# Optimization experiments

Hardware: AMD Instinct MI355X
Metric: run time of the kernel (lower is better)

The kernel has to match this reference:

```python
import jax, jax.numpy as jnp
import numpy as np

D_MODEL = 1024
N_HEADS = 16
D_K = D_MODEL // N_HEADS
MAX_REL = 128
SEQ = 1024
BATCH = 4


def setup_inputs() -> dict:
    key = jax.random.key(0)
    ks = jax.random.split(key, 8)
    x = jax.random.normal(ks[0], (SEQ, BATCH, D_MODEL), dtype=jnp.float32)
    # nn.Linear weights: shape (out, in), applied as x @ W.T
    w_q = jax.random.normal(ks[1], (D_MODEL, D_MODEL), dtype=jnp.float32) * (1.0 / np.sqrt(D_MODEL))
    w_k = jax.random.normal(ks[2], (D_MODEL, D_MODEL), dtype=jnp.float32) * (1.0 / np.sqrt(D_MODEL))
    w_v = jax.random.normal(ks[3], (D_MODEL, D_MODEL), dtype=jnp.float32) * (1.0 / np.sqrt(D_MODEL))
    w_o = jax.random.normal(ks[4], (D_MODEL, D_MODEL), dtype=jnp.float32) * (1.0 / np.sqrt(D_MODEL))
    b_o = jnp.zeros((D_MODEL,), dtype=jnp.float32)
    rel_k = jax.random.normal(ks[5], (2 * MAX_REL + 1, D_K), dtype=jnp.float32)
    rel_v = jax.random.normal(ks[6], (2 * MAX_REL + 1, D_K), dtype=jnp.float32)
    return {"x": x, "w_q": w_q, "w_k": w_k, "w_v": w_v, "w_o": w_o, "b_o": b_o,
            "rel_k": rel_k, "rel_v": rel_v}


def _relative_positions(seq_len: int) -> jnp.ndarray:
    pos = jnp.arange(seq_len)
    rel = pos[:, None] - pos[None, :]
    rel = jnp.clip(rel, -MAX_REL, MAX_REL) + MAX_REL
    return rel  # [s, t] int indices into relative tables


def reference(x, w_q, w_k, w_v, w_o, b_o, rel_k, rel_v):
    seq_len, batch, _ = x.shape
    scale = 1.0 / np.sqrt(D_K)
    Q = (x @ w_q.T).reshape(seq_len, batch, N_HEADS, D_K)
    K = (x @ w_k.T).reshape(seq_len, batch, N_HEADS, D_K)
    V = (x @ w_v.T).reshape(seq_len, batch, N_HEADS, D_K)

    rel_idx = _relative_positions(seq_len)          # [s, t]
    rk = rel_k[rel_idx]                              # [s, t, d_k]
    rv = rel_v[rel_idx]                              # [s, t, d_k]

    scores = jnp.einsum('sbhd,tbhd->sbth', Q, K) * scale
    scores = scores + jnp.einsum('sbhd,std->sbth', Q, rk) * scale
    # NOTE: original torch code softmaxes over dim=-1 of [s,b,t,h], i.e. the
    # head axis; reproduced faithfully here.
    attn = jax.nn.softmax(scores, axis=-1)           # [s, b, t, h]

    out = jnp.einsum('sbth,tbhd->sbhd', attn, V)
    out = out + jnp.einsum('sbth,std->sbhd', attn, rv)
    out = out.reshape(seq_len, batch, D_MODEL)
    return out @ w_o.T + b_o
```

## Files before the change

kernel.cpp:

```cpp
#include <hip/hip_runtime.h>
#include <stdint.h>

#define DI __device__ __forceinline__

typedef __attribute__((ext_vector_type(8))) short bfx8;
typedef __attribute__((ext_vector_type(4))) short bfx4;
typedef __attribute__((ext_vector_type(4))) float f4;

DI unsigned short f2bf(float x){
  unsigned u = __float_as_uint(x);
  u = (u + 0x7FFFu + ((u >> 16) & 1u)) >> 16;
  return (unsigned short)u;
}
DI float bf2f(unsigned short h){ return __uint_as_float(((unsigned)h) << 16); }

DI f4 mfma32(bfx8 a, bfx8 b, f4 c){
  return __builtin_amdgcn_mfma_f32_16x16x32_bf16(a, b, c, 0, 0, 0);
}
#if __has_builtin(__builtin_amdgcn_mfma_f32_16x16x16bf16_1k)
DI f4 mfma16(bfx4 a, bfx4 b, f4 c){
  return __builtin_amdgcn_mfma_f32_16x16x16bf16_1k(a, b, c, 0, 0, 0);
}
#else
DI f4 mfma16(bfx4 a, bfx4 b, f4 c){
  f4 d = c;
  asm volatile("v_mfma_f32_16x16x16_bf16 %0, %1, %2, %0" : "+v"(d) : "v"(a), "v"(b));
  return d;
}
#endif

DI bfx4 lo4(bfx8 v){ bfx4 r; r[0]=v[0]; r[1]=v[1]; r[2]=v[2]; r[3]=v[3]; return r; }
DI bfx4 hi4(bfx8 v){ bfx4 r; r[0]=v[4]; r[1]=v[5]; r[2]=v[6]; r[3]=v[7]; return r; }

DI void gload16(const void* g, void* l){
  __builtin_amdgcn_global_load_lds(
      (__attribute__((address_space(1))) void*)g,
      (__attribute__((address_space(3))) void*)l, 16, 0, 0);
}


__global__ void k_cast(const float* __restrict__ src, unsigned short* __restrict__ dst, int n4){
  int i = blockIdx.x*256 + threadIdx.x;
  if (i < n4){
    const float4 v = ((const float4*)src)[i];
    bfx4 o;
    o[0] = (short)f2bf(v.x); o[1] = (short)f2bf(v.y);
    o[2] = (short)f2bf(v.z); o[3] = (short)f2bf(v.w);
    *(bfx4*)(dst + (size_t)i*4) = o;
  }
}

__global__ void k_castw(const float* __restrict__ s0, const float* __restrict__ s1,
                        const float* __restrict__ s2, const float* __restrict__ s3,
                        unsigned short* __restrict__ dst){
  int i = blockIdx.x*256 + threadIdx.x;
  const float* src = (blockIdx.y==0) ? s0 : (blockIdx.y==1) ? s1 : (blockIdx.y==2) ? s2 : s3;
  const float4 v = ((const float4*)src)[i];
  bfx4 o;
  o[0] = (short)f2bf(v.x); o[1] = (short)f2bf(v.y);
  o[2] = (short)f2bf(v.z); o[3] = (short)f2bf(v.w);
  *(bfx4*)(dst + (size_t)blockIdx.y*1048576 + (size_t)i*4) = o;
}

__global__ void k_relprep(const float* __restrict__ rlk, const float* __restrict__ rlv,
                          unsigned short* __restrict__ relk_bf, unsigned short* __restrict__ relvT_bf){
  int i = blockIdx.x*256 + threadIdx.x;
  if (i < 272*64){
    int r = i >> 6, d = i & 63;
    relk_bf[i] = (r < 257) ? f2bf(rlk[r*64 + d]) : (unsigned short)0;
  }
  if (i < 64*288){
    int d = i / 288, r = i % 288;
    relvT_bf[i] = (r < 257) ? f2bf(rlv[(size_t)r*64 + d]) : (unsigned short)0;
  }
}

__global__ __launch_bounds__(256, 3) void k_qkv(
    const unsigned short* __restrict__ xbf, const unsigned short* __restrict__ wqkv,
    unsigned short* __restrict__ Qf, unsigned short* __restrict__ Kf,
    unsigned short* __restrict__ Vf)
{
  __shared__ __align__(16) unsigned short smem[2][8192];
  const int nt = blockIdx.x;
  const int b  = blockIdx.y;
  const int st = blockIdx.z;
  const int w = threadIdx.x >> 6, lane = threadIdx.x & 63;
  const int wr = w >> 1, wc = w & 1;
  const int p = lane & 15, g = lane >> 4;
  const int s0 = st*128;
  const int n0 = nt*128;
  const f4 fz = {0.f,0.f,0.f,0.f};
  f4 acc[4][4];
#pragma unroll
  for (int m=0;m<4;++m)
#pragma unroll
    for (int n=0;n<4;++n) acc[m][n] = fz;

  const int j0 = w*2, j1 = w*2 + 1;
  const unsigned short* gA = xbf  + (size_t)((s0 + p)*4 + b)*1024 + g*8;
  const unsigned short* gB = wqkv + (size_t)(n0 + p)*1024 + g*8;

  {
    unsigned short* d0 = &smem[0][0];
    gload16(gA + (size_t)j0*65536, d0 + j0*512);
    gload16(gA + (size_t)j1*65536, d0 + j1*512);
    gload16(gB + (size_t)j0*16384, d0 + 4096 + j0*512);
    gload16(gB + (size_t)j1*16384, d0 + 4096 + j1*512);
  }

  for (int it=0; it<32; ++it){
    const int cur = it & 1;
    if (it < 31){
      const int kn = (it+1)*32;
      unsigned short* dn = &smem[cur^1][0];
      gload16(gA + (size_t)j0*65536 + kn, dn + j0*512);
      gload16(gA + (size_t)j1*65536 + kn, dn + j1*512);
      gload16(gB + (size_t)j0*16384 + kn, dn + 4096 + j0*512);
      gload16(gB + (size_t)j1*16384 + kn, dn + 4096 + j1*512);
      asm volatile("s_waitcnt vmcnt(4)" ::: "memory");
    } else {
      asm volatile("s_waitcnt vmcnt(0)" ::: "memory");
    }
    __builtin_amdgcn_sched_barrier(0);
    __builtin_amdgcn_s_barrier();
    __builtin_amdgcn_sched_barrier(0);
    {
      const unsigned short* Ab = &smem[cur][0];
      bfx8 af[4], bfr[4];
#pragma unroll
      for (int m=0;m<4;++m) af[m] = *(const bfx8*)(Ab + (wr*4+m)*512 + lane*8);
#pragma unroll
      for (int n=0;n<4;++n) bfr[n] = *(const bfx8*)(Ab + 4096 + (wc*4+n)*512 + lane*8);
#pragma unroll
      for (int m=0;m<4;++m)
#pragma unroll
        for (int n=0;n<4;++n)
          acc[m][n] = mfma32(af[m], bfr[n], acc[m][n]);
    }
    __builtin_amdgcn_sched_barrier(0);
    __builtin_amdgcn_s_barrier();
    __builtin_amdgcn_sched_barrier(0);
  }

  const int n64 = n0 + wc*64;
  const int sec = n64 >> 10;
  const int h = (n64 & 1023) >> 6;
  float* es = (float*)&smem[0][0] + w*1280;

  if (sec < 2){
    const float scl = (sec == 0) ? 0.125f : 1.0f;
    unsigned short* dst = (sec == 0) ? Qf : Kf;
#pragma unroll
    for (int m=0;m<4;++m){
#pragma unroll
      for (int n=0;n<4;++n)
#pragma unroll
        for (int r=0;r<4;++r)
          es[(4*g + r)*80 + 16*n + p] = acc[m][n][r] * scl;
      __syncthreads();
      f4 v0 = *(const f4*)&es[p*80 + 8*g];
      f4 v1 = *(const f4*)&es[p*80 + 8*g + 4];
      f4 v2 = *(const f4*)&es[p*80 + 32 + 8*g];
      f4 v3 = *(const f4*)&es[p*80 + 32 + 8*g + 4];
      bfx8 lo, hi;
#pragma unroll
      for (int j=0;j<4;++j){
        lo[j]   = (short)f2bf(v0[j]);
        lo[j+4] = (short)f2bf(v1[j]);
        hi[j]   = (short)f2bf(v2[j]);
        hi[j+4] = (short)f2bf(v3[j]);
      }
      size_t fb = ((size_t)(b*16 + h)*64 + (st*8 + wr*4 + m))*1024 + (size_t)lane*16;
      *(bfx8*)(dst + fb) = lo;
      *(bfx8*)(dst + fb + 8) = hi;
      __syncthreads();
    }
  } else {
#pragma unroll
    for (int m=0;m<4;++m){
#pragma unroll
      for (int n=0;n<4;++n)
        *(f4*)&es[(16*n + p)*20 + 4*g] = acc[m][n];
      __syncthreads();
      f4 vv0 = *(const f4*)&es[(p)*20 + 4*g];
      f4 vv1 = *(const f4*)&es[(16 + p)*20 + 4*g];
      f4 vv2 = *(const f4*)&es[(32 + p)*20 + 4*g];
      f4 vv3 = *(const f4*)&es[(48 + p)*20 + 4*g];
      bfx8 lo, hi;
#pragma unroll
      for (int j=0;j<4;++j){
        lo[j]   = (short)f2bf(vv0[j]);
        lo[j+4] = (short)f2bf(vv1[j]);
        hi[j]   = (short)f2bf(vv2[j]);
        hi[j+4] = (short)f2bf(vv3[j]);
      }
      size_t fb = ((size_t)(b*16 + h)*64 + (st*8 + wr*4 + m))*1024 + (size_t)lane*16;
      *(bfx8*)(Vf + fb) = lo;
      *(bfx8*)(Vf + fb + 8) = hi;
      __syncthreads();
    }
  }
}

__global__ __launch_bounds__(256) void k_qr(
    const unsigned short* __restrict__ Qf, const unsigned short* __restrict__ relk,
    unsigned short* __restrict__ Qr2)
{
  __shared__ __align__(16) unsigned short sst[16][16][24];
  const int bx = blockIdx.x;
  const int b  = bx & 3;
  const int st = (bx >> 2) & 63;
  const int uh = bx >> 8;
  const int w = threadIdx.x >> 6, lane = threadIdx.x & 63;
  const int p = lane & 15, g = lane >> 4;
  const int s0 = st << 4;
  const f4 fz = {0.f,0.f,0.f,0.f};

  bfx8 a0[4], a1[4];
#pragma unroll
  for (int hh=0; hh<4; ++hh){
    size_t fb = (((size_t)(b*16 + w*4 + hh))*64 + st)*1024 + (size_t)lane*16;
    a0[hh] = *(const bfx8*)(Qf + fb);
    a1[hh] = *(const bfx8*)(Qf + fb + 8);
  }

  const int c0 = uh ? 9 : 0;
  const int c1 = uh ? 17 : 9;
  const int so = threadIdx.x >> 4, uo = threadIdx.x & 15;

  for (int c=c0; c<c1; ++c){
    const int r0 = c << 4;
    bfx8 b0 = *(const bfx8*)(relk + (size_t)(r0 + p)*64 + 8*g);
    bfx8 b1 = *(const bfx8*)(relk + (size_t)(r0 + p)*64 + 32 + 8*g);
#pragma unroll
    for (int hh=0; hh<4; ++hh){
      f4 acc = mfma32(a1[hh], b1, mfma32(a0[hh], b0, fz));
#pragma unroll
      for (int r=0; r<4; ++r)
        sst[4*g + r][p][w*4 + hh] = f2bf(acc[r]);
    }
    __syncthreads();
    bfx8 v0 = *(const bfx8*)&sst[so][uo][0];
    bfx8 v1 = *(const bfx8*)&sst[so][uo][8];
    size_t ga = (((size_t)b*1024 + s0 + so)*272 + r0 + uo)*16;
    *(bfx8*)(Qr2 + ga) = v0;
    *(bfx8*)(Qr2 + ga + 8) = v1;
    __syncthreads();
  }
}

__global__ __launch_bounds__(512, 4) void k_s(
    const unsigned short* __restrict__ Qf, const unsigned short* __restrict__ Kf,
    const unsigned short* __restrict__ Qr2, float* __restrict__ ivf)
{
  __shared__ __align__(16) unsigned short qs[2][2][1024];
  __shared__ __align__(16) unsigned short ks[2][4][1024];
  const int pbid = blockIdx.x;
  const int b   = pbid & 3;
  const int ttg = (pbid >> 2) & 15;
  const int stg = pbid >> 6;
  const int w = threadIdx.x >> 6, lane = threadIdx.x & 63;
  const int stl = w >> 2, ttl = w & 3;
  const int st = stg*2 + stl;
  const int tt = ttg*4 + ttl;
  const int p = lane & 15, g = lane >> 4;
  const int s = (st << 4) + p;
  const int t0 = tt << 4;
  const f4 fz = {0.f,0.f,0.f,0.f};

  bfx8 rv[4][2];
#pragma unroll
  for (int r=0; r<4; ++r){
    int t = t0 + 4*g + r;
    int u = s - t + 128; u = u < 0 ? 0 : (u > 256 ? 256 : u);
    const unsigned short* q = Qr2 + (((size_t)b*1024 + s)*272 + u)*16;
    rv[r][0] = *(const bfx8*)q;
    rv[r][1] = *(const bfx8*)(q + 8);
  }

  const bool stager = (w <= 1) || (w >= 4);
  const unsigned short* gsrc =
      (w <= 1) ? (Qf + ((size_t)(b*16)*64 + (stg*2 + w))*1024)
               : (Kf + ((size_t)(b*16)*64 + (ttg*4 + (w & 3)))*1024);
  unsigned short* ldst[2];
  ldst[0] = (w <= 1) ? &qs[0][w][0] : &ks[0][w & 3][0];
  ldst[1] = (w <= 1) ? &qs[1][w][0] : &ks[1][w & 3][0];

  if (stager){
    gload16(gsrc + (size_t)lane*8, ldst[0]);
    gload16(gsrc + 512 + (size_t)lane*8, ldst[0] + 512);
    asm volatile("s_waitcnt vmcnt(0)" ::: "memory");
  }
  __builtin_amdgcn_sched_barrier(0);
  __builtin_amdgcn_s_barrier();
  __builtin_amdgcn_sched_barrier(0);

  f4 ps = fz;
#pragma unroll
  for (int h=0; h<16; ++h){
    const int buf = h & 1;
    if (h < 15 && stager){
      unsigned short* ld = ldst[buf ^ 1];
      gload16(gsrc + (size_t)(h+1)*65536 + (size_t)lane*8, ld);
      gload16(gsrc + (size_t)(h+1)*65536 + 512 + (size_t)lane*8, ld + 512);
    }
    {
      const unsigned short* qb = &qs[buf][stl][lane*16];
      const unsigned short* kb = &ks[buf][ttl][lane*16];
      bfx8 q0 = *(const bfx8*)qb;
      bfx8 q1 = *(const bfx8*)(qb + 8);
      bfx8 k0 = *(const bfx8*)kb;
      bfx8 k1 = *(const bfx8*)(kb + 8);
      f4 sc = mfma32(k1, q1, mfma32(k0, q0, fz));
      const int hg = h >> 3, hr = h & 7;
#pragma unroll
      for (int r=0; r<4; ++r)
        ps[r] += __expf(sc[r] + bf2f((unsigned short)rv[r][hg][hr]));
    }
    if (h < 15){
      if (stager) asm volatile("s_waitcnt vmcnt(0)" ::: "memory");
      __builtin_amdgcn_sched_barrier(0);
      __builtin_amdgcn_s_barrier();
      __builtin_amdgcn_sched_barrier(0);
    }
  }

  f4 inv;
#pragma unroll
  for (int r=0; r<4; ++r) inv[r] = 1.0f / ps[r];
  *(f4*)(ivf + (((size_t)(b*64 + tt)*64 + st)*64 + lane)*4) = inv;
}

__global__ __launch_bounds__(256, 2) void k_attn(
    const unsigned short* __restrict__ Qf, const unsigned short* __restrict__ Kf,
    const unsigned short* __restrict__ Vf, const unsigned short* __restrict__ Qr2,
    const float* __restrict__ ivf, const unsigned short* __restrict__ relvT,
    const float* __restrict__ relv, unsigned short* __restrict__ out1)
{
  __shared__ __align__(16) unsigned short skew[128*264];
  const int pbid = blockIdx.x;
  const int xcd = pbid & 7;
  const int b = xcd >> 1;
  const int hhalf = (pbid >> 3) & 1;
  const int st = ((pbid >> 4) << 1) | (xcd & 1);
  const int s0 = st << 4;
  const int w = threadIdx.x >> 6;
  const int lane = threadIdx.x & 63;
  const int p = lane & 15, g = lane >> 4;
  const int s = s0 + p;
  const int hl0 = w * 2;
  const int h0 = hhalf*8 + hl0;
  const f4 fz = {0.f,0.f,0.f,0.f};

  {
    unsigned* zp = (unsigned*)skew + w*4224;
    for (int i = lane; i < 4224; i += 64) zp[i] = 0u;
  }

  bfx8 qf[2][2]; float qr0[2], qr1[2];
#pragma unroll
  for (int hh=0; hh<2; ++hh){
    size_t qb = (((size_t)(b*16 + h0 + hh))*64 + st)*1024 + (size_t)lane*16;
    qf[hh][0] = *(const bfx8*)(Qf + qb);
    qf[hh][1] = *(const bfx8*)(Qf + qb + 8);
    qr0[hh] = bf2f(Qr2[(((size_t)b*1024 + s)*272 + 0)*16 + (h0+hh)]);
    qr1[hh] = bf2f(Qr2[(((size_t)b*1024 + s)*272 + 256)*16 + (h0+hh)]);
  }

  f4 o[2][4];
#pragma unroll
  for (int hh=0; hh<2; ++hh)
#pragma unroll
    for (int df=0; df<4; ++df) o[hh][df] = fz;

  float tl0[2] = {0.f,0.f};
  float tl1[2] = {0.f,0.f};

  const int tlo = (st-8 < 0) ? 0 : st-8;
  const int thi = (st+8 > 63) ? 63 : st+8;

  bfx8 kc[2][2]; bfx8 vc8[2][2]; unsigned short qc[2][4]; f4 is;
  bfx8 kn[2][2]; bfx8 vn8[2][2]; unsigned short qn[2][4]; f4 isn;

#pragma unroll
  for (int hh=0; hh<2; ++hh){
    size_t bh = (size_t)(b*16 + h0 + hh);
    size_t fb = (bh*64 + 0)*1024 + (size_t)lane*16;
    kc[hh][0] = *(const bfx8*)(Kf + fb);
    kc[hh][1] = *(const bfx8*)(Kf + fb + 8);
    vc8[hh][0] = *(const bfx8*)(Vf + fb);
    vc8[hh][1] = *(const bfx8*)(Vf + fb + 8);
  }
  if (0 >= tlo){
#pragma unroll
    for (int hh=0; hh<2; ++hh)
#pragma unroll
      for (int r=0; r<4; ++r){
        int t = 4*g + r;
        int u = s - t + 128; u = u < 0 ? 0 : (u > 256 ? 256 : u);
        qc[hh][r] = Qr2[(((size_t)b*1024 + s)*272 + u)*16 + (h0+hh)];
      }
  }
  is = *(const f4*)(ivf + (((size_t)(b*64 + 0)*64 + st)*64 + lane)*4);

  for (int ti = 0; ti < 64; ++ti){
    const int t0 = ti << 4;
    const bool nearT = (ti >= tlo) && (ti <= thi);

    if (ti < 63){
      const int tn = ti + 1;
#pragma unroll
      for (int hh=0; hh<2; ++hh){
        size_t bh = (size_t)(b*16 + h0 + hh);
        size_t fb = (bh*64 + tn)*1024 + (size_t)lane*16;
        kn[hh][0] = *(const bfx8*)(Kf + fb);
        kn[hh][1] = *(const bfx8*)(Kf + fb + 8);
        vn8[hh][0] = *(const bfx8*)(Vf + fb);
        vn8[hh][1] = *(const bfx8*)(Vf + fb + 8);
      }
      if (tn >= tlo && tn <= thi){
#pragma unroll
        for (int hh=0; hh<2; ++hh)
#pragma unroll
          for (int r=0; r<4; ++r){
            int t = (tn<<4) + 4*g + r;
            int u = s - t + 128; u = u < 0 ? 0 : (u > 256 ? 256 : u);
            qn[hh][r] = Qr2[(((size_t)b*1024 + s)*272 + u)*16 + (h0+hh)];
          }
      }
      isn = *(const f4*)(ivf + (((size_t)(b*64 + tn)*64 + st)*64 + lane)*4);
    }

    if (nearT){
#pragma unroll
      for (int hh=0; hh<2; ++hh){
        f4 sc = mfma32(kc[hh][1], qf[hh][1], mfma32(kc[hh][0], qf[hh][0], fz));
        f4 at;
#pragma unroll
        for (int r=0; r<4; ++r) at[r] = __expf(sc[r] + bf2f(qc[hh][r])) * is[r];
        const int row = (hl0 + hh)*16 + p;
#pragma unroll
        for (int r=0; r<4; ++r){
          int t = t0 + 4*g + r;
          int u = s - t + 128;
          float a = at[r];
          if (u <= 0) tl0[hh] += a;
          else if (u >= 256) tl1[hh] += a;
          else skew[row*264 + u] = f2bf(a);
        }
        bfx4 pk;
#pragma unroll
        for (int r=0; r<4; ++r) pk[r] = (short)f2bf(at[r]);
        o[hh][0] = mfma16(lo4(vc8[hh][0]), pk, o[hh][0]);
        o[hh][1] = mfma16(hi4(vc8[hh][0]), pk, o[hh][1]);
        o[hh][2] = mfma16(lo4(vc8[hh][1]), pk, o[hh][2]);
        o[hh][3] = mfma16(hi4(vc8[hh][1]), pk, o[hh][3]);
      }
    } else {
      const bool hiSide = (ti < st);
#pragma unroll
      for (int hh=0; hh<2; ++hh){
        f4 sc = mfma32(kc[hh][1], qf[hh][1], mfma32(kc[hh][0], qf[hh][0], fz));
        const float qa = hiSide ? qr1[hh] : qr0[hh];
        f4 at;
#pragma unroll
        for (int r=0; r<4; ++r) at[r] = __expf(sc[r] + qa) * is[r];
        float tsum = at[0] + at[1] + at[2] + at[3];
        if (hiSide) tl1[hh] += tsum; else tl0[hh] += tsum;
        bfx4 pk;
#pragma unroll
        for (int r=0; r<4; ++r) pk[r] = (short)f2bf(at[r]);
        o[hh][0] = mfma16(lo4(vc8[hh][0]), pk, o[hh][0]);
        o[hh][1] = mfma16(hi4(vc8[hh][0]), pk, o[hh][1]);
        o[hh][2] = mfma16(lo4(vc8[hh][1]), pk, o[hh][2]);
        o[hh][3] = mfma16(hi4(vc8[hh][1]), pk, o[hh][3]);
      }
    }

    if (ti < 63){
#pragma unroll
      for (int hh=0; hh<2; ++hh){
#pragma unroll
        for (int kf=0; kf<2; ++kf){ kc[hh][kf] = kn[hh][kf]; vc8[hh][kf] = vn8[hh][kf]; }
#pragma unroll
        for (int r=0; r<4; ++r) qc[hh][r] = qn[hh][r];
      }
      is = isn;
    }
  }

  __syncthreads();

  f4 acc2[2][4];
#pragma unroll
  for (int hh=0; hh<2; ++hh)
#pragma unroll
    for (int df=0; df<4; ++df) acc2[hh][df] = fz;
#pragma unroll
  for (int k0=0; k0<256; k0+=32){
    bfx8 bb0 = *(const bfx8*)&skew[(hl0*16 + p)*264 + k0 + 8*g];
    bfx8 bb1 = *(const bfx8*)&skew[((hl0+1)*16 + p)*264 + k0 + 8*g];
#pragma unroll
    for (int df=0; df<4; ++df){
      bfx8 a = *(const bfx8*)(relvT + (size_t)(df*16 + p)*288 + k0 + 8*g);
      acc2[0][df] = mfma32(a, bb0, acc2[0][df]);
      acc2[1][df] = mfma32(a, bb1, acc2[1][df]);
    }
  }

  f4 rv0[4], rv1[4];
#pragma unroll
  for (int df=0; df<4; ++df){
    rv0[df] = *(const f4*)(relv + df*16 + 4*g);
    rv1[df] = *(const f4*)(relv + 16384 + df*16 + 4*g);
  }
#pragma unroll
  for (int hh=0; hh<2; ++hh){
    float tv0 = tl0[hh];
    tv0 += __shfl_xor(tv0, 16, 64);
    tv0 += __shfl_xor(tv0, 32, 64);
    float tv1 = tl1[hh];
    tv1 += __shfl_xor(tv1, 16, 64);
    tv1 += __shfl_xor(tv1, 32, 64);
#pragma unroll
    for (int df=0; df<4; ++df)
#pragma unroll
      for (int r=0; r<4; ++r)
        o[hh][df][r] += acc2[hh][df][r] + tv0*rv0[df][r] + tv1*rv1[df][r];
  }

  __syncthreads();

  float* slabBase = (float*)skew;
  float (*tb)[68] = (float(*)[68])(slabBase + w*(16*68));
#pragma unroll
  for (int hh=0; hh<2; ++hh){
#pragma unroll
    for (int df=0; df<4; ++df)
      *(f4*)&tb[p][df*16 + 4*g] = o[hh][df];
    __syncthreads();
    const int srow = lane >> 2, quad = lane & 3;
    f4 r0 = *(const f4*)&tb[srow][quad*16 + 0];
    f4 r1 = *(const f4*)&tb[srow][quad*16 + 4];
    f4 r2 = *(const f4*)&tb[srow][quad*16 + 8];
    f4 r3 = *(const f4*)&tb[srow][quad*16 + 12];
    size_t addr = ((size_t)b*1024 + s0 + srow)*1024 + (h0+hh)*64 + quad*16;
    bfx8 pa, pb;
#pragma unroll
    for (int j=0; j<4; ++j){
      pa[j]   = (short)f2bf(r0[j]);
      pa[j+4] = (short)f2bf(r1[j]);
      pb[j]   = (short)f2bf(r2[j]);
      pb[j+4] = (short)f2bf(r3[j]);
    }
    *(bfx8*)(out1 + addr) = pa;
    *(bfx8*)(out1 + addr + 8) = pb;
    __syncthreads();
  }
}

__global__ __launch_bounds__(256) void k_wo(
    const unsigned short* __restrict__ out1, const unsigned short* __restrict__ wo,
    const float* __restrict__ bo, float* __restrict__ dout)
{
  __shared__ __align__(16) unsigned short smem[2][6144];
  const int nt = blockIdx.x;
  const int mt = blockIdx.y;
  const int w = threadIdx.x >> 6, lane = threadIdx.x & 63;
  const int wr = w >> 1, wc = w & 1;
  const int p = lane & 15, g = lane >> 4;
  const int m0 = mt*64, n0 = nt*128;
  const f4 fz = {0.f,0.f,0.f,0.f};
  f4 acc[2][4];
#pragma unroll
  for (int m=0;m<2;++m)
#pragma unroll
    for (int n=0;n<4;++n) acc[m][n] = fz;

  const int j0 = w*2, j1 = w*2 + 1;
  const unsigned short* gA = out1 + (size_t)(m0 + p)*1024 + g*8;
  const unsigned short* gB = wo   + (size_t)(n0 + p)*1024 + g*8;

  {
    unsigned short* d0 = &smem[0][0];
    gload16(gA + (size_t)w*16384, d0 + w*512);
    gload16(gB + (size_t)j0*16384, d0 + 2048 + j0*512);
    gload16(gB + (size_t)j1*16384, d0 + 2048 + j1*512);
  }

  for (int it=0; it<32; ++it){
    const int cur = it & 1;
    if (it < 31){
      const int kn = (it+1)*32;
      unsigned short* dn = &smem[cur^1][0];
      gload16(gA + (size_t)w*16384 + kn, dn + w*512);
      gload16(gB + (size_t)j0*16384 + kn, dn + 2048 + j0*512);
      gload16(gB + (size_t)j1*16384 + kn, dn + 2048 + j1*512);
      asm volatile("s_waitcnt vmcnt(3)" ::: "memory");
    } else {
      asm volatile("s_waitcnt vmcnt(0)" ::: "memory");
    }
    __builtin_amdgcn_sched_barrier(0);
    __builtin_amdgcn_s_barrier();
    __builtin_amdgcn_sched_barrier(0);
    {
      const unsigned short* Ab = &smem[cur][0];
      bfx8 af[2], bfr[4];
#pragma unroll
      for (int m=0;m<2;++m) af[m] = *(const bfx8*)(Ab + (wr*2+m)*512 + lane*8);
#pragma unroll
      for (int n=0;n<4;++n) bfr[n] = *(const bfx8*)(Ab + 2048 + (wc*4+n)*512 + lane*8);
#pragma unroll
      for (int m=0;m<2;++m)
#pragma unroll
        for (int n=0;n<4;++n)
          acc[m][n] = mfma32(af[m], bfr[n], acc[m][n]);
    }
    __builtin_amdgcn_sched_barrier(0);
    __builtin_amdgcn_s_barrier();
    __builtin_amdgcn_sched_barrier(0);
  }

#pragma unroll
  for (int n=0;n<4;++n){
    const int col = n0 + wc*64 + n*16 + p;
    const float bias = bo[col];
#pragma unroll
    for (int m=0;m<2;++m)
#pragma unroll
      for (int r=0;r<4;++r){
        int row = m0 + wr*32 + m*16 + 4*g + r;
        int bb = row >> 10, s = row & 1023;
        dout[((size_t)s*4 + bb)*1024 + col] = acc[m][n][r] + bias;
      }
  }
}

extern "C" void kernel_launch(void* const* d_in, const int* in_sizes, int n_in,
                              void* d_out, int out_size, void* d_ws, size_t ws_size,
                              hipStream_t stream){
  const float* x   = (const float*)d_in[0];
  const float* wq  = (const float*)d_in[1];
  const float* wk  = (const float*)d_in[2];
  const float* wv  = (const float*)d_in[3];
  const float* wo  = (const float*)d_in[4];
  const float* bo  = (const float*)d_in[5];
  const float* rlk = (const float*)d_in[6];
  const float* rlv = (const float*)d_in[7];
  char* ws = (char*)d_ws;

  unsigned short* x_bf    = (unsigned short*)(ws + 0);
  unsigned short* wq_bf   = (unsigned short*)(ws + 8388608);
  unsigned short* relk_bf = (unsigned short*)(ws + 16777216);
  unsigned short* relvT_bf= (unsigned short*)(ws + 16812032);
  unsigned short* Qf      = (unsigned short*)(ws + 16848896);
  unsigned short* Kf      = (unsigned short*)(ws + 25237504);
  unsigned short* Vf      = (unsigned short*)(ws + 33626112);
  unsigned short* Qr2     = (unsigned short*)(ws + 42014720);
  unsigned short* out1    = (unsigned short*)(ws + 113317888);
  float*          ivf     = (float*)        (ws + 121706496);
  unsigned short* wo_bf   = (unsigned short*)(ws + 14680064);

  k_cast<<<4096, 256, 0, stream>>>(x, x_bf, 1048576);
  k_castw<<<dim3(1024,4), 256, 0, stream>>>(wq, wk, wv, wo, wq_bf);
  k_relprep<<<72, 256, 0, stream>>>(rlk, rlv, relk_bf, relvT_bf);

  k_qkv<<<dim3(24,4,8), 256, 0, stream>>>(x_bf, wq_bf, Qf, Kf, Vf);
  k_qr<<<512, 256, 0, stream>>>(Qf, relk_bf, Qr2);

  k_s   <<<2048, 512, 0, stream>>>(Qf, Kf, Qr2, ivf);
  k_attn<<<512, 256, 0, stream>>>(Qf, Kf, Vf, Qr2, ivf, relvT_bf, rlv, out1);
  k_wo<<<dim3(8,64), 256, 0, stream>>>(out1, wo_bf, bo, (float*)d_out);
}
```

Before: 223.9 us.

## Merge prep casts into one kernel, use packed bf16 convert, raise qkv occupancy

Fuses the three input/weight/relative-table cast kernels into a single launch to remove two kernel launches and their gaps. In the attention kernel, the per-element software bf16 rounding is replaced with the hardware v_cvt_pk_bf16_f32 instruction, which packs two values per instruction. The k_qkv launch bound goes from 3 to 4 waves-per-SIMD minimum, which may force register spilling. The hardware convert's rounding should match round-to-nearest-even but may differ on NaN handling.

```diff
diff --git a/kernel.cpp b/kernel.cpp
--- a/kernel.cpp
+++ b/kernel.cpp
@@ -13,6 +13,12 @@
   return (unsigned short)u;
 }
 DI float bf2f(unsigned short h){ return __uint_as_float(((unsigned)h) << 16); }
+
+DI unsigned cvtpk(float lo, float hi){
+  unsigned r;
+  asm("v_cvt_pk_bf16_f32 %0, %1, %2" : "=v"(r) : "v"(lo), "v"(hi));
+  return r;
+}
 
 DI f4 mfma32(bfx8 a, bfx8 b, f4 c){
   return __builtin_amdgcn_mfma_f32_16x16x32_bf16(a, b, c, 0, 0, 0);
@@ -39,43 +45,43 @@
 }
 
 
-__global__ void k_cast(const float* __restrict__ src, unsigned short* __restrict__ dst, int n4){
-  int i = blockIdx.x*256 + threadIdx.x;
-  if (i < n4){
+__global__ void k_prep(const float* __restrict__ x,
+                       const float* __restrict__ wq, const float* __restrict__ wk,
+                       const float* __restrict__ wv, const float* __restrict__ wo,
+                       const float* __restrict__ rlk, const float* __restrict__ rlv,
+                       unsigned short* __restrict__ x_bf, unsigned short* __restrict__ w_bf,
+                       unsigned short* __restrict__ relk_bf, unsigned short* __restrict__ relvT_bf){
+  const int bid = blockIdx.x;
+  if (bid < 4096){
+    int i = bid*256 + threadIdx.x;
+    const float4 v = ((const float4*)x)[i];
+    bfx4 o;
+    o[0] = (short)f2bf(v.x); o[1] = (short)f2bf(v.y);
+    o[2] = (short)f2bf(v.z); o[3] = (short)f2bf(v.w);
+    *(bfx4*)(x_bf + (size_t)i*4) = o;
+  } else if (bid < 8192){
+    const int wb = (bid - 4096) >> 10;
+    const float* src = (wb==0) ? wq : (wb==1) ? wk : (wb==2) ? wv : wo;
+    int i = ((bid - 4096) & 1023)*256 + threadIdx.x;
     const float4 v = ((const float4*)src)[i];
     bfx4 o;
     o[0] = (short)f2bf(v.x); o[1] = (short)f2bf(v.y);
     o[2] = (short)f2bf(v.z); o[3] = (short)f2bf(v.w);
-    *(bfx4*)(dst + (size_t)i*4) = o;
-  }
-}
-
-__global__ void k_castw(const float* __restrict__ s0, const float* __restrict__ s1,
-                        const float* __restrict__ s2, const float* __restrict__ s3,
-                        unsigned short* __restrict__ dst){
-  int i = blockIdx.x*256 + threadIdx.x;
-  const float* src = (blockIdx.y==0) ? s0 : (blockIdx.y==1) ? s1 : (blockIdx.y==2) ? s2 : s3;
-  const float4 v = ((const float4*)src)[i];
-  bfx4 o;
-  o[0] = (short)f2bf(v.x); o[1] = (short)f2bf(v.y);
-  o[2] = (short)f2bf(v.z); o[3] = (short)f2bf(v.w);
-  *(bfx4*)(dst + (size_t)blockIdx.y*1048576 + (size_t)i*4) = o;
-}
-
-__global__ void k_relprep(const float* __restrict__ rlk, const float* __restrict__ rlv,
-                          unsigned short* __restrict__ relk_bf, unsigned short* __restrict__ relvT_bf){
-  int i = blockIdx.x*256 + threadIdx.x;
-  if (i < 272*64){
-    int r = i >> 6, d = i & 63;
-    relk_bf[i] = (r < 257) ? f2bf(rlk[r*64 + d]) : (unsigned short)0;
-  }
-  if (i < 64*288){
-    int d = i / 288, r = i % 288;
-    relvT_bf[i] = (r < 257) ? f2bf(rlv[(size_t)r*64 + d]) : (unsigned short)0;
-  }
-}
-
-__global__ __launch_bounds__(256, 3) void k_qkv(
+    *(bfx4*)(w_bf + (size_t)wb*1048576 + (size_t)i*4) = o;
+  } else {
+    int i = (bid - 8192)*256 + threadIdx.x;
+    if (i < 272*64){
+      int r = i >> 6, d = i & 63;
+      relk_bf[i] = (r < 257) ? f2bf(rlk[r*64 + d]) : (unsigned short)0;
+    }
+    if (i < 64*288){
+      int d = i / 288, r = i % 288;
+      relvT_bf[i] = (r < 257) ? f2bf(rlv[(size_t)r*64 + d]) : (unsigned short)0;
+    }
+  }
+}
+
+__global__ __launch_bounds__(256, 4) void k_qkv(
     const unsigned short* __restrict__ xbf, const unsigned short* __restrict__ wqkv,
     unsigned short* __restrict__ Qf, unsigned short* __restrict__ Kf,
     unsigned short* __restrict__ Vf)
@@ -438,19 +444,23 @@
         f4 at;
 #pragma unroll
         for (int r=0; r<4; ++r) at[r] = __expf(sc[r] + bf2f(qc[hh][r])) * is[r];
+        const unsigned w0 = cvtpk(at[0], at[1]);
+        const unsigned w1 = cvtpk(at[2], at[3]);
+        const unsigned short abf[4] = {
+          (unsigned short)(w0 & 0xffffu), (unsigned short)(w0 >> 16),
+          (unsigned short)(w1 & 0xffffu), (unsigned short)(w1 >> 16) };
         const int row = (hl0 + hh)*16 + p;
 #pragma unroll
         for (int r=0; r<4; ++r){
           int t = t0 + 4*g + r;
           int u = s - t + 128;
-          float a = at[r];
-          if (u <= 0) tl0[hh] += a;
-          else if (u >= 256) tl1[hh] += a;
-          else skew[row*264 + u] = f2bf(a);
+          if (u <= 0) tl0[hh] += at[r];
+          else if (u >= 256) tl1[hh] += at[r];
+          else skew[row*264 + u] = abf[r];
         }
-        bfx4 pk;
-#pragma unroll
-        for (int r=0; r<4; ++r) pk[r] = (short)f2bf(at[r]);
+        union { unsigned u[2]; bfx4 v; } cv;
+        cv.u[0] = w0; cv.u[1] = w1;
+        const bfx4 pk = cv.v;
         o[hh][0] = mfma16(lo4(vc8[hh][0]), pk, o[hh][0]);
         o[hh][1] = mfma16(hi4(vc8[hh][0]), pk, o[hh][1]);
         o[hh][2] = mfma16(lo4(vc8[hh][1]), pk, o[hh][2]);
@@ -467,9 +477,11 @@
         for (int r=0; r<4; ++r) at[r] = __expf(sc[r] + qa) * is[r];
         float tsum = at[0] + at[1] + at[2] + at[3];
         if (hiSide) tl1[hh] += tsum; else tl0[hh] += tsum;
-        bfx4 pk;
-#pragma unroll
-        for (int r=0; r<4; ++r) pk[r] = (short)f2bf(at[r]);
+        const unsigned w0 = cvtpk(at[0], at[1]);
+        const unsigned w1 = cvtpk(at[2], at[3]);
+        union { unsigned u[2]; bfx4 v; } cv;
+        cv.u[0] = w0; cv.u[1] = w1;
+        const bfx4 pk = cv.v;
         o[hh][0] = mfma16(lo4(vc8[hh][0]), pk, o[hh][0]);
         o[hh][1] = mfma16(hi4(vc8[hh][0]), pk, o[hh][1]);
         o[hh][2] = mfma16(lo4(vc8[hh][1]), pk, o[hh][2]);
@@ -661,9 +673,8 @@
   float*          ivf     = (float*)        (ws + 121706496);
   unsigned short* wo_bf   = (unsigned short*)(ws + 14680064);
 
-  k_cast<<<4096, 256, 0, stream>>>(x, x_bf, 1048576);
-  k_castw<<<dim3(1024,4), 256, 0, stream>>>(wq, wk, wv, wo, wq_bf);
-  k_relprep<<<72, 256, 0, stream>>>(rlk, rlv, relk_bf, relvT_bf);
+  k_prep<<<8264, 256, 0, stream>>>(x, wq, wk, wv, wo, rlk, rlv,
+                                   x_bf, wq_bf, relk_bf, relvT_bf);
 
   k_qkv<<<dim3(24,4,8), 256, 0, stream>>>(x_bf, wq_bf, Qf, Kf, Vf);
   k_qr<<<512, 256, 0, stream>>>(Qf, relk_bf, Qr2);
```

Measured after the change: 218.1 us. -2.6%, faster.
